# Performance work log

Measured on AMD Instinct MI355X. Metric: run time of the kernel, lower is better.

Reference implementation:

```python
import jax, jax.numpy as jnp
import numpy as np

B, K, N, D, H, NNEG, NTOP = 8, 8, 128, 256, 128, 64, 64
UNARY_SCALES = (1.0, 1.0, 1.0)  # one scale per tree level, tree_height = log2(K) = 3


def setup_inputs():
    key = jax.random.key(0)
    ks = jax.random.split(key, 8)
    s = 0.05
    return {
        'pos_fea': jax.random.normal(ks[0], (B, K, N, D), jnp.float32),
        'neg_fea': jax.random.normal(ks[1], (B * K, NNEG, D), jnp.float32),
        'pos_classes': jax.random.randint(ks[2], (B, K, N), 0, 20),
        'target_class': jax.random.randint(ks[3], (B,), 0, 20),
        'Wp1': jax.random.normal(ks[4], (2 * D, H), jnp.float32) * s,
        'bp1': jnp.zeros((H,), jnp.float32),
        'Wp2': jax.random.normal(ks[5], (H, 1), jnp.float32) * s,
        'bp2': jnp.zeros((1,), jnp.float32),
        'Wu1': jax.random.normal(ks[6], (2 * D, H), jnp.float32) * s,
        'bu1': jnp.zeros((H,), jnp.float32),
        'Wu2': jax.random.normal(ks[7], (H, 1), jnp.float32) * s,
        'bu2': jnp.zeros((1,), jnp.float32),
    }


def _relation(f0, f1, W1, b1, W2, b2):
    # RelationModule: Dense(H, relu) -> Dense(1) applied to concat([f0_m, f1_n])
    # for every cross pair; concat-Dense is split into two GEMMs. -> [Bn, M0, M1]
    d = f0.shape[-1]
    h0 = jnp.einsum('bmd,dh->bmh', f0, W1[:d])
    h1 = jnp.einsum('bnd,dh->bnh', f1, W1[d:])
    h = jax.nn.relu(h0[:, :, None, :] + h1[:, None, :, :] + b1)
    return jnp.einsum('bmnh,h->bmn', h, W2[:, 0]) + b2[0]


def _bg(t, idx):
    # batched_gather along axis 1: t [Bn, P, ...], idx [Bn, T]
    ie = idx.reshape(idx.shape + (1,) * (t.ndim - 2))
    ie = jnp.broadcast_to(ie, idx.shape + t.shape[2:])
    return jnp.take_along_axis(t, ie, axis=1)


def _rep(fea, sub):
    # subproblem representative feature: fea [Bn,S,N,D], sub [Bn,M,S] -> [Bn,M,D]
    idx = jnp.swapaxes(sub, 1, 2)[..., None]              # [Bn,S,M,1]
    idx = jnp.broadcast_to(idx, idx.shape[:-1] + (fea.shape[-1],))
    return jnp.take_along_axis(fea, idx, axis=2).mean(axis=1)


def _tree(pos_fea, neg_fea, Wp1, bp1, Wp2, bp2, Wu1, bu1, Wu2, bu2):
    pos_flat = pos_fea.reshape(B * K, N, D)
    # UnaryModule: mean relation score of each positive proposal vs the negative bag
    ue = _relation(pos_flat, neg_fea, Wu1, bu1, Wu2, bu2).mean(-1)   # [B*K, N]
    sub = jnp.broadcast_to(jnp.arange(N, dtype=jnp.int32)[None, :, None], (B * K, N, 1))
    pe = jnp.zeros_like(ue)
    tree_height = int(np.log2(K))
    best = None
    for i in range(tree_height):
        S = 2 ** i                      # subproblem size per branch at this level
        Bn = sub.shape[0] // 2
        M = sub.shape[1]
        sub2 = sub.reshape(Bn, 2, M, S)  # [::2] / [1::2] split of adjacent rows
        sub0, sub1 = sub2[:, 0], sub2[:, 1]
        pe2 = pe.reshape(Bn, 2, M)
        ue2 = ue.reshape(Bn, 2, M)
        fea = pos_flat.reshape(Bn, 2, S, N, D)
        rep0 = _rep(fea[:, 0], sub0)
        rep1 = _rep(fea[:, 1], sub1)
        # PairwiseCrossSimilarity: scores for all cross pairs of candidates
        scores = _relation(rep0, rep1, Wp1, bp1, Wp2, bp2).reshape(Bn, M * M)
        p0 = jnp.repeat(jnp.arange(M), M)
        p1 = jnp.tile(jnp.arange(M), M)
        pe = pe2[:, 0][:, p0] + pe2[:, 1][:, p1] - scores
        ue = ue2[:, 0][:, p0] + ue2[:, 1][:, p1]
        total = pe + UNARY_SCALES[i] * ue
        sub = jnp.concatenate([sub0[:, p0], sub1[:, p1]], axis=-1)  # [Bn, M*M, 2S]
        topk = 1 if i == tree_height - 1 else min(M * M, NTOP)
        _, inds = jax.lax.top_k(-total, topk)
        sub = _bg(sub, inds)
        ue = jnp.take_along_axis(ue, inds, axis=1)
        pe = jnp.take_along_axis(pe, inds, axis=1)
        best = jnp.take_along_axis(total, inds, axis=1)
    return sub, best


def reference(pos_fea, neg_fea, pos_classes, target_class,
              Wp1, bp1, Wp2, bp2, Wu1, bu1, Wu2, bu2):
    sub, _ = _tree(pos_fea, neg_fea, Wp1, bp1, Wp2, bp2, Wu1, bu1, Wu2, bu2)
    is_target = (pos_classes == target_class[:, None, None]).astype(jnp.float32)
    return sub[:, 0], is_target  # selected proposal per image [B,K], [B,K,N]
```

## Files before the change

kernel.cpp:

```cpp
#include <hip/hip_runtime.h>
#include <stdint.h>

#define B_ 8
#define K_ 8
#define N_ 128
#define D_ 256
#define H_ 128
#define NNEG_ 64

typedef unsigned long long u64;

__device__ __forceinline__ u64 shfl_xor_u64(u64 v, int m) {
    int lo = __shfl_xor((int)(unsigned)v, m, 64);
    int hi = __shfl_xor((int)(unsigned)(v >> 32), m, 64);
    return ((u64)(unsigned)hi << 32) | (unsigned)lo;
}
__device__ __forceinline__ u64 bitonic_merge64(u64 m, int lane) {
#pragma unroll
    for (int j = 32; j > 0; j >>= 1) {
        u64 o = shfl_xor_u64(m, j);
        bool keepMin = ((lane & j) == 0);
        bool lt = m < o;
        m = (keepMin == lt) ? m : o;
    }
    return m;
}
__device__ __forceinline__ u64 merge2(u64 a, u64 b, int lane) {
    u64 br = shfl_xor_u64(b, 63);
    u64 m = a < br ? a : br;
    return bitonic_merge64(m, lane);
}
__device__ __forceinline__ unsigned sortable(float f) {
    unsigned u = __float_as_uint(f);
    return (u & 0x80000000u) ? ~u : (u | 0x80000000u);
}
__device__ __forceinline__ float unsortable(unsigned u) {
    return __uint_as_float((u & 0x80000000u) ? (u & 0x7FFFFFFFu) : ~u);
}
__device__ __forceinline__ void sort128_reg(u64& v0, u64& v1, int lane) {
#pragma unroll
    for (int k = 2; k <= 64; k <<= 1) {
        bool d0 = ((lane & k) == 0);
        bool d1 = (k == 64) ? false : d0;
#pragma unroll
        for (int j = k >> 1; j > 0; j >>= 1) {
            u64 o0 = shfl_xor_u64(v0, j);
            bool km0 = (((lane & j) == 0) == d0);
            v0 = (km0 == (v0 < o0)) ? v0 : o0;
            u64 o1 = shfl_xor_u64(v1, j);
            bool km1 = (((lane & j) == 0) == d1);
            v1 = (km1 == (v1 < o1)) ? v1 : o1;
        }
    }
    if (v0 > v1) { u64 tmp = v0; v0 = v1; v1 = tmp; }
#pragma unroll
    for (int j = 32; j > 0; j >>= 1) {
        bool km = ((lane & j) == 0);
        u64 o0 = shfl_xor_u64(v0, j);
        v0 = (km == (v0 < o0)) ? v0 : o0;
        u64 o1 = shfl_xor_u64(v1, j);
        v1 = (km == (v1 < o1)) ? v1 : o1;
    }
}

__global__ __launch_bounds__(128) void g1_gemm(
    const float* __restrict__ pos, const float* __restrict__ neg,
    const float* __restrict__ Wu1, const float* __restrict__ Wp1,
    const int* __restrict__ pos_classes, const int* __restrict__ target_class,
    float* __restrict__ HU0, float* __restrict__ HU1n,
    float* __restrict__ HP0, float* __restrict__ HP1,
    float* __restrict__ outp) {
    int bid = blockIdx.x;
    int t = threadIdx.x;
    if (bid >= 896) {
        int base = (bid - 896) * 2048 + t * 16;
#pragma unroll
        for (int q = 0; q < 16; ++q) {
            int idx = base + q;
            outp[64 + idx] = (pos_classes[idx] == target_class[idx >> 10]) ? 1.0f : 0.0f;
        }
        return;
    }
    const float* A; const float* W; float* OUT; int bid2;
    if (bid < 256)      { A = pos; W = Wu1;           OUT = HU0;  bid2 = bid; }
    else if (bid < 384) { A = neg; W = Wu1 + D_ * H_; OUT = HU1n; bid2 = bid - 256; }
    else if (bid < 640) { A = pos; W = Wp1;           OUT = HP0;  bid2 = bid - 384; }
    else                { A = pos; W = Wp1 + D_ * H_; OUT = HP1;  bid2 = bid - 640; }
    int rb = (bid2 >> 1) * 64;
    int cb64 = (bid2 & 1) * 64;

    __shared__ float AsT[2][32][68];
    __shared__ float Bs[2][32][64];
    int tx = t & 7, ty = t >> 3;
    float acc[4][8];
#pragma unroll
    for (int i = 0; i < 4; ++i)
#pragma unroll
        for (int j = 0; j < 8; ++j) acc[i][j] = 0.f;

#pragma unroll
    for (int rep = 0; rep < 4; ++rep) {
        int flat = t + rep * 128;
        int row = flat >> 3, kq = flat & 7;
        const float4 av = *(const float4*)&A[(size_t)(rb + row) * D_ + kq * 4];
        AsT[0][kq * 4 + 0][row] = av.x;
        AsT[0][kq * 4 + 1][row] = av.y;
        AsT[0][kq * 4 + 2][row] = av.z;
        AsT[0][kq * 4 + 3][row] = av.w;
    }
#pragma unroll
    for (int rep = 0; rep < 4; ++rep) {
        int flat = t + rep * 128;
        int kr = flat >> 4, cq = flat & 15;
        *(float4*)&Bs[0][kr][cq * 4] =
            *(const float4*)&W[(size_t)kr * H_ + cb64 + cq * 4];
    }
    __syncthreads();

    for (int chunk = 0; chunk < 8; ++chunk) {
        int cur = chunk & 1, nxt = cur ^ 1;
        bool pre = (chunk < 7);
        int k0n = (chunk + 1) * 32;
        float4 pa[4], pb[4];
        if (pre) {
#pragma unroll
            for (int rep = 0; rep < 4; ++rep) {
                int flat = t + rep * 128;
                int row = flat >> 3, kq = flat & 7;
                pa[rep] = *(const float4*)&A[(size_t)(rb + row) * D_ + k0n + kq * 4];
            }
#pragma unroll
            for (int rep = 0; rep < 4; ++rep) {
                int flat = t + rep * 128;
                int kr = flat >> 4, cq = flat & 15;
                pb[rep] = *(const float4*)&W[(size_t)(k0n + kr) * H_ + cb64 + cq * 4];
            }
        }
#pragma unroll 8
        for (int kk = 0; kk < 32; ++kk) {
            const float4 av = *(const float4*)&AsT[cur][kk][ty * 4];
            float bv[8];
            *(float4*)&bv[0] = *(const float4*)&Bs[cur][kk][tx * 8];
            *(float4*)&bv[4] = *(const float4*)&Bs[cur][kk][tx * 8 + 4];
#pragma unroll
            for (int j = 0; j < 8; ++j) {
                acc[0][j] += av.x * bv[j];
                acc[1][j] += av.y * bv[j];
                acc[2][j] += av.z * bv[j];
                acc[3][j] += av.w * bv[j];
            }
        }
        if (pre) {
#pragma unroll
            for (int rep = 0; rep < 4; ++rep) {
                int flat = t + rep * 128;
                int row = flat >> 3, kq = flat & 7;
                AsT[nxt][kq * 4 + 0][row] = pa[rep].x;
                AsT[nxt][kq * 4 + 1][row] = pa[rep].y;
                AsT[nxt][kq * 4 + 2][row] = pa[rep].z;
                AsT[nxt][kq * 4 + 3][row] = pa[rep].w;
            }
#pragma unroll
            for (int rep = 0; rep < 4; ++rep) {
                int flat = t + rep * 128;
                int kr = flat >> 4, cq = flat & 15;
                *(float4*)&Bs[nxt][kr][cq * 4] = pb[rep];
            }
        }
        __syncthreads();
    }
#pragma unroll
    for (int i = 0; i < 4; ++i) {
        float4 o0 = {acc[i][0], acc[i][1], acc[i][2], acc[i][3]};
        float4 o1 = {acc[i][4], acc[i][5], acc[i][6], acc[i][7]};
        *(float4*)&OUT[(size_t)(rb + ty * 4 + i) * H_ + cb64 + tx * 8] = o0;
        *(float4*)&OUT[(size_t)(rb + ty * 4 + i) * H_ + cb64 + tx * 8 + 4] = o1;
    }
}

__global__ __launch_bounds__(256) void g2_ue_sc0(
    const float* __restrict__ HU0, const float* __restrict__ HU1n,
    const float* __restrict__ bu1, const float* __restrict__ Wu2,
    const float* __restrict__ bu2v,
    const float* __restrict__ HP0, const float* __restrict__ HP1,
    const float* __restrict__ bp1, const float* __restrict__ Wp2,
    const float* __restrict__ bp2,
    float* __restrict__ t0, float* __restrict__ sc0) {
    __shared__ float LsT[128][36];
    __shared__ float RsT[128][66];
    __shared__ float wsv[128];
    __shared__ float red[32][33];

    int bid = blockIdx.x;
    int t = threadIdx.x;
    bool is_ue = bid < 256;

    const float* Lsrc; const float* Rsrc; const float* b1v; const float* W2;
    if (is_ue) {
        int bk = bid >> 2, mt = bid & 3;
        Lsrc = HU0 + (size_t)(bk * N_ + mt * 32) * H_;
        Rsrc = HU1n + (size_t)bk * NNEG_ * H_;
        b1v = bu1; W2 = Wu2;
    } else {
        int bid2 = bid - 256;
        int b = bid2 >> 3, m0t = (bid2 >> 1) & 3, m1t = bid2 & 1;
        Lsrc = HP0 + (size_t)b * 2 * N_ * H_ + m0t * 32 * H_;
        Rsrc = HP1 + (size_t)b * 2 * N_ * H_ + N_ * H_ + m1t * 64 * H_;
        b1v = bp1; W2 = Wp2;
    }
    for (int i = t; i < 32 * 32; i += 256) {
        int m = i & 31, hq = i >> 5;
        const float4 a = *(const float4*)&Lsrc[(size_t)m * H_ + hq * 4];
        const float4 b = *(const float4*)&b1v[hq * 4];
        LsT[hq * 4 + 0][m] = a.x + b.x;
        LsT[hq * 4 + 1][m] = a.y + b.y;
        LsT[hq * 4 + 2][m] = a.z + b.z;
        LsT[hq * 4 + 3][m] = a.w + b.w;
    }
    for (int i = t; i < 64 * 32; i += 256) {
        int n = i & 63, hq = i >> 6;
        const float4 a = *(const float4*)&Rsrc[(size_t)n * H_ + hq * 4];
        RsT[hq * 4 + 0][n] = a.x;
        RsT[hq * 4 + 1][n] = a.y;
        RsT[hq * 4 + 2][n] = a.z;
        RsT[hq * 4 + 3][n] = a.w;
    }
    if (t < 128) wsv[t] = W2[t];
    __syncthreads();

    int tm = t & 7, tn = t >> 3;
    float a00 = 0.f, a01 = 0.f, a10 = 0.f, a11 = 0.f;
    float a20 = 0.f, a21 = 0.f, a30 = 0.f, a31 = 0.f;
#pragma unroll 4
    for (int h = 0; h < 128; ++h) {
        const float4 lv = *(const float4*)&LsT[h][tm * 4];
        const float2 rv = *(const float2*)&RsT[h][tn * 2];
        float w = wsv[h];
        float v;
        v = lv.x + rv.x; v = v > 0.f ? v : 0.f; a00 += v * w;
        v = lv.x + rv.y; v = v > 0.f ? v : 0.f; a01 += v * w;
        v = lv.y + rv.x; v = v > 0.f ? v : 0.f; a10 += v * w;
        v = lv.y + rv.y; v = v > 0.f ? v : 0.f; a11 += v * w;
        v = lv.z + rv.x; v = v > 0.f ? v : 0.f; a20 += v * w;
        v = lv.z + rv.y; v = v > 0.f ? v : 0.f; a21 += v * w;
        v = lv.w + rv.x; v = v > 0.f ? v : 0.f; a30 += v * w;
        v = lv.w + rv.y; v = v > 0.f ? v : 0.f; a31 += v * w;
    }

    if (is_ue) {
        int bk = bid >> 2, mt = bid & 3;
        red[tm * 4 + 0][tn] = a00 + a01;
        red[tm * 4 + 1][tn] = a10 + a11;
        red[tm * 4 + 2][tn] = a20 + a21;
        red[tm * 4 + 3][tn] = a30 + a31;
        __syncthreads();
        if (t < 32) {
            float s = 0.f;
            for (int q = 0; q < 32; ++q) s += red[t][q];
            t0[bk * N_ + mt * 32 + t] = s * (1.0f / NNEG_) + bu2v[0];
        }
    } else {
        int bid2 = bid - 256;
        int b = bid2 >> 3, m0t = (bid2 >> 1) & 3, m1t = bid2 & 1;
        float bp2v = bp2[0];
        float* orow = sc0 + (size_t)b * 16384;
        float accs[4][2] = {{a00, a01}, {a10, a11}, {a20, a21}, {a30, a31}};
#pragma unroll
        for (int i = 0; i < 4; ++i) {
            int m0 = m0t * 32 + tm * 4 + i;
#pragma unroll
            for (int j = 0; j < 2; ++j) {
                int m1 = m1t * 64 + tn * 2 + j;
                orow[m0 * 128 + m1] = accs[i][j] + bp2v;
            }
        }
    }
}

__global__ __launch_bounds__(256) void g3a_top0(const float* __restrict__ sc0,
                                                const float* __restrict__ t0,
                                                u64* __restrict__ g3c) {
    int bid = blockIdx.x;
    int r = bid >> 3, c = bid & 7;
    int t = threadIdx.x, lane = t & 63, w = t >> 6;
    __shared__ float tt[256];
    __shared__ u64 cand[4][128];
    if (t < 256) tt[t] = t0[r * 256 + t];
    __syncthreads();
    const float* row = sc0 + (size_t)r * 16384 + c * 2048 + w * 512;
    unsigned sv[8];
#pragma unroll
    for (int j = 0; j < 8; ++j) {
        int li = j * 64 + lane;
        int idx = c * 2048 + w * 512 + li;
        float v = (tt[idx >> 7] + tt[128 + (idx & 127)]) - row[li];
        sv[j] = sortable(v);
    }
    unsigned T = 0u;
#pragma unroll
    for (int it = 0; it < 16; ++it) {
        int p = 30 - 2 * it;
        unsigned C1 = T | (1u << p), C2 = T | (2u << p), C3 = T | (3u << p);
        unsigned c1 = 0u, c2 = 0u, c3 = 0u;
#pragma unroll
        for (int j = 0; j < 8; ++j) {
            c1 += (unsigned)__popcll(__ballot(sv[j] < C1));
            c2 += (unsigned)__popcll(__ballot(sv[j] < C2));
            c3 += (unsigned)__popcll(__ballot(sv[j] < C3));
        }
        unsigned k = (c3 < 64u) ? 3u : (c2 < 64u) ? 2u : (c1 < 64u) ? 1u : 0u;
        T |= (k << p);
    }
    u64* my = cand[w];
    int base = 0;
#pragma unroll
    for (int j = 0; j < 8; ++j) {
        u64 mask = __ballot(sv[j] <= T);
        if (sv[j] <= T) {
            int pos = base + (int)__popcll(mask & ((1ull << lane) - 1ull));
            if (pos < 128) {
                int idx = c * 2048 + w * 512 + j * 64 + lane;
                my[pos] = ((u64)sv[j] << 32) | (unsigned)idx;
            }
        }
        base += (int)__popcll(mask);
    }
    int cc = base < 128 ? base : 128;
    u64 v0 = (lane < cc) ? my[lane] : ~0ull;
    u64 v1 = (64 + lane < cc) ? my[64 + lane] : ~0ull;
    sort128_reg(v0, v1, lane);
    my[lane] = v0;
    __syncthreads();
    if (w == 0) {
        u64 x0 = cand[0][lane], x1 = cand[1][lane];
        u64 x2 = cand[2][lane], x3 = cand[3][lane];
        u64 y0 = merge2(x0, x1, lane), y1 = merge2(x2, x3, lane);
        g3c[(size_t)bid * 64 + lane] = merge2(y0, y1, lane);
    }
}

__global__ __launch_bounds__(256) void g4a_s1(
    const float* __restrict__ HP0, const float* __restrict__ HP1,
    const u64* __restrict__ g3c, int* __restrict__ pA,
    const float* __restrict__ bp1, const float* __restrict__ Wp2,
    const float* __restrict__ bp2, u64* __restrict__ g4top) {
    int bid = blockIdx.x;
    int u = bid >> 3, mq = (bid >> 1) & 3, nh = bid & 1;
    int t = threadIdx.x, lane = t & 63, w = t >> 6;
    __shared__ float LsT[128][17];
    __shared__ float RsT[128][34];
    __shared__ float taL[64], taR[64];
    __shared__ int paL[64], paR[64];
    __shared__ float wsv[128];
    __shared__ u64 cand[4][64];
    if (w < 2) {
        const u64* Lp = g3c + (size_t)(2 * u + w) * 512;
        u64 x0 = Lp[lane], x1 = Lp[64 + lane], x2 = Lp[128 + lane], x3 = Lp[192 + lane];
        u64 x4 = Lp[256 + lane], x5 = Lp[320 + lane], x6 = Lp[384 + lane], x7 = Lp[448 + lane];
        u64 y0 = merge2(x0, x1, lane), y1 = merge2(x2, x3, lane);
        u64 y2 = merge2(x4, x5, lane), y3 = merge2(x6, x7, lane);
        u64 z0 = merge2(y0, y1, lane), z1 = merge2(y2, y3, lane);
        u64 f = merge2(z0, z1, lane);
        int idx = (int)(f & 0xFFFFFFFFull);
        int pk = ((idx >> 7) << 8) | (idx & 127);
        float tv = unsortable((unsigned)(f >> 32));
        if (w == 0) { taL[lane] = tv; paL[lane] = pk; }
        else        { taR[lane] = tv; paR[lane] = pk; }
    }
    if (t >= 128) wsv[t - 128] = Wp2[t - 128];
    float bp2v = bp2[0];
    __syncthreads();
    if ((bid & 7) == 0) {
        if (t < 64) pA[(2 * u) * 64 + t] = paL[t];
        else if (t < 128) pA[(2 * u + 1) * 64 + (t - 64)] = paR[t - 64];
    }
    for (int i = t; i < 16 * 128; i += 256) {
        int m = i >> 7, h = i & 127;
        int pk = paL[mq * 16 + m]; int a0 = pk >> 8, a1 = pk & 255;
        float s = HP0[(size_t)(4 * u) * 16384 + a0 * 128 + h]
                + HP0[(size_t)(4 * u + 1) * 16384 + a1 * 128 + h];
        LsT[h][m] = s * 0.5f + bp1[h];
    }
    for (int i = t; i < 32 * 128; i += 256) {
        int n = i >> 7, h = i & 127;
        int pk = paR[nh * 32 + n]; int c0 = pk >> 8, c1 = pk & 255;
        float s = HP1[(size_t)(4 * u + 2) * 16384 + c0 * 128 + h]
                + HP1[(size_t)(4 * u + 3) * 16384 + c1 * 128 + h];
        RsT[h][n] = s * 0.5f;
    }
    __syncthreads();
    int lm = w * 4 + (lane >> 4);
    int ln = lane & 15;
    float a0 = 0.f, a1 = 0.f;
#pragma unroll 4
    for (int h = 0; h < 128; ++h) {
        float lv = LsT[h][lm];
        const float2 rv = *(const float2*)&RsT[h][ln * 2];
        float wv = wsv[h];
        float v;
        v = lv + rv.x; v = v > 0.f ? v : 0.f; a0 += v * wv;
        v = lv + rv.y; v = v > 0.f ? v : 0.f; a1 += v * wv;
    }
    int m_unit = mq * 16 + lm;
    int n0 = nh * 32 + ln * 2;
    float val0 = (taL[mq * 16 + lm] + taR[nh * 32 + ln * 2 + 0]) - (a0 + bp2v);
    float val1 = (taL[mq * 16 + lm] + taR[nh * 32 + ln * 2 + 1]) - (a1 + bp2v);
    u64 v0 = ((u64)sortable(val0) << 32) | (unsigned)(m_unit * 64 + n0);
    u64 v1 = ((u64)sortable(val1) << 32) | (unsigned)(m_unit * 64 + n0 + 1);
    sort128_reg(v0, v1, lane);
    cand[w][lane] = v0;
    __syncthreads();
    if (w == 0) {
        u64 x0 = cand[0][lane], x1 = cand[1][lane];
        u64 x2 = cand[2][lane], x3 = cand[3][lane];
        u64 y0 = merge2(x0, x1, lane), y1 = merge2(x2, x3, lane);
        g4top[(size_t)bid * 64 + lane] = merge2(y0, y1, lane);
    }
}

__global__ __launch_bounds__(256) void g4b_s2(
    const float* __restrict__ HP0, const float* __restrict__ HP1,
    const int* __restrict__ pA, const u64* __restrict__ g4top,
    const float* __restrict__ bp1, const float* __restrict__ Wp2,
    const float* __restrict__ bp2, float* __restrict__ outp) {
    int b = blockIdx.x;
    int t = threadIdx.x, lane = t & 63, w = t >> 6;
    __shared__ float LsT[128][68];
    __shared__ float RsT[128][36];
    __shared__ float tL[64], tR[64];
    __shared__ unsigned subL[64], subR[64];
    __shared__ float wsv[128];
    __shared__ u64 sred[4];
    if (t < 128) wsv[t] = Wp2[t];
    float bp2v = bp2[0];
    if (w < 2) {
        const u64* Lp = g4top + (size_t)(2 * b + w) * 512;
        u64 x0 = Lp[lane], x1 = Lp[64 + lane], x2 = Lp[128 + lane], x3 = Lp[192 + lane];
        u64 x4 = Lp[256 + lane], x5 = Lp[320 + lane], x6 = Lp[384 + lane], x7 = Lp[448 + lane];
        u64 y0 = merge2(x0, x1, lane), y1 = merge2(x2, x3, lane);
        u64 y2 = merge2(x4, x5, lane), y3 = merge2(x6, x7, lane);
        u64 z0 = merge2(y0, y1, lane), z1 = merge2(y2, y3, lane);
        u64 m = merge2(z0, z1, lane);
        int idx = (int)(m & 0xFFFFFFFFull);
        int p0 = idx >> 6, p1 = idx & 63;
        float val = unsortable((unsigned)(m >> 32));
        int rowL = 4 * b + 2 * w;
        int pkL = pA[rowL * 64 + p0];
        int pkR = pA[(rowL + 1) * 64 + p1];
        unsigned leaves = ((unsigned)pkL << 16) | (unsigned)pkR;
        if (w == 0) { tL[lane] = val; subL[lane] = leaves; }
        else        { tR[lane] = val; subR[lane] = leaves; }
    }
    __syncthreads();
    for (int i = t; i < 64 * 128; i += 256) {
        int m = i >> 7, h = i & 127;
        unsigned s4 = subL[m];
        float s = HP0[(size_t)(8 * b + 0) * 16384 + ((s4 >> 24) & 255u) * 128 + h]
                + HP0[(size_t)(8 * b + 1) * 16384 + ((s4 >> 16) & 255u) * 128 + h]
                + HP0[(size_t)(8 * b + 2) * 16384 + ((s4 >> 8) & 255u) * 128 + h]
                + HP0[(size_t)(8 * b + 3) * 16384 + (s4 & 255u) * 128 + h];
        LsT[h][m] = s * 0.25f + bp1[h];
    }
    u64 best = ~0ull;
    int qm = w * 4 + (lane >> 4);
    int qn = lane & 15;
    for (int half = 0; half < 2; ++half) {
        __syncthreads();
        for (int i = t; i < 32 * 128; i += 256) {
            int n = i >> 7, h = i & 127;
            int ng = half * 32 + n;
            unsigned s4 = subR[ng];
            float s = HP1[(size_t)(8 * b + 4) * 16384 + ((s4 >> 24) & 255u) * 128 + h]
                    + HP1[(size_t)(8 * b + 5) * 16384 + ((s4 >> 16) & 255u) * 128 + h]
                    + HP1[(size_t)(8 * b + 6) * 16384 + ((s4 >> 8) & 255u) * 128 + h]
                    + HP1[(size_t)(8 * b + 7) * 16384 + (s4 & 255u) * 128 + h];
            RsT[h][n] = s * 0.25f;
        }
        __syncthreads();
        float acc[4][2];
#pragma unroll
        for (int i = 0; i < 4; ++i) { acc[i][0] = 0.f; acc[i][1] = 0.f; }
#pragma unroll 2
        for (int h = 0; h < 128; ++h) {
            const float4 lv = *(const float4*)&LsT[h][qm * 4];
            const float2 rv = *(const float2*)&RsT[h][qn * 2];
            float wv = wsv[h];
            float v;
            v = lv.x + rv.x; v = v > 0.f ? v : 0.f; acc[0][0] += v * wv;
            v = lv.x + rv.y; v = v > 0.f ? v : 0.f; acc[0][1] += v * wv;
            v = lv.y + rv.x; v = v > 0.f ? v : 0.f; acc[1][0] += v * wv;
            v = lv.y + rv.y; v = v > 0.f ? v : 0.f; acc[1][1] += v * wv;
            v = lv.z + rv.x; v = v > 0.f ? v : 0.f; acc[2][0] += v * wv;
            v = lv.z + rv.y; v = v > 0.f ? v : 0.f; acc[2][1] += v * wv;
            v = lv.w + rv.x; v = v > 0.f ? v : 0.f; acc[3][0] += v * wv;
            v = lv.w + rv.y; v = v > 0.f ? v : 0.f; acc[3][1] += v * wv;
        }
#pragma unroll
        for (int mi = 0; mi < 4; ++mi) {
#pragma unroll
            for (int nj = 0; nj < 2; ++nj) {
                int m = qm * 4 + mi;
                int ng = half * 32 + qn * 2 + nj;
                float val = (tL[m] + tR[ng]) - (acc[mi][nj] + bp2v);
                u64 kk = ((u64)sortable(val) << 32) | (unsigned)(m * 64 + ng);
                best = kk < best ? kk : best;
            }
        }
    }
#pragma unroll
    for (int off = 32; off > 0; off >>= 1) {
        u64 o = shfl_xor_u64(best, off);
        best = o < best ? o : best;
    }
    if (lane == 0) sred[w] = best;
    __syncthreads();
    if (t == 0) {
        u64 bb = sred[0];
        for (int p = 1; p < 4; ++p) { u64 o = sred[p]; bb = o < bb ? o : bb; }
        int idx = (int)(bb & 0xFFFFFFFFull);
        unsigned sl = subL[idx >> 6], sr = subR[idx & 63];
        outp[b * 8 + 0] = (float)((sl >> 24) & 255u);
        outp[b * 8 + 1] = (float)((sl >> 16) & 255u);
        outp[b * 8 + 2] = (float)((sl >> 8) & 255u);
        outp[b * 8 + 3] = (float)(sl & 255u);
        outp[b * 8 + 4] = (float)((sr >> 24) & 255u);
        outp[b * 8 + 5] = (float)((sr >> 16) & 255u);
        outp[b * 8 + 6] = (float)((sr >> 8) & 255u);
        outp[b * 8 + 7] = (float)(sr & 255u);
    }
}

extern "C" void kernel_launch(void* const* d_in, const int* in_sizes, int n_in,
                              void* d_out, int out_size, void* d_ws, size_t ws_size,
                              hipStream_t stream) {
    const float* pos = (const float*)d_in[0];
    const float* neg = (const float*)d_in[1];
    const int* pos_classes = (const int*)d_in[2];
    const int* target_class = (const int*)d_in[3];
    const float* Wp1 = (const float*)d_in[4];
    const float* bp1 = (const float*)d_in[5];
    const float* Wp2 = (const float*)d_in[6];
    const float* bp2 = (const float*)d_in[7];
    const float* Wu1 = (const float*)d_in[8];
    const float* bu1 = (const float*)d_in[9];
    const float* Wu2 = (const float*)d_in[10];
    const float* bu2 = (const float*)d_in[11];

    float* wsf = (float*)d_ws;
    float* HU0 = wsf;
    float* HP0 = HU0 + 1048576;
    float* HP1 = HP0 + 1048576;
    float* HU1n = HP1 + 1048576;
    float* t0 = HU1n + 524288;
    float* sc0 = t0 + 8192;
    int* pA = (int*)(sc0 + 524288);
    u64* g3c = (u64*)wsf;
    u64* g4top = (u64*)wsf + 16384;
    float* outp = (float*)d_out;

    g1_gemm<<<900, 128, 0, stream>>>(pos, neg, Wu1, Wp1, pos_classes,
                                     target_class, HU0, HU1n, HP0, HP1, outp);
    g2_ue_sc0<<<512, 256, 0, stream>>>(HU0, HU1n, bu1, Wu2, bu2,
                                       HP0, HP1, bp1, Wp2, bp2, t0, sc0);
    g3a_top0<<<256, 256, 0, stream>>>(sc0, t0, g3c);
    g4a_s1<<<128, 256, 0, stream>>>(HP0, HP1, g3c, pA, bp1, Wp2, bp2, g4top);
    g4b_s2<<<8, 256, 0, stream>>>(HP0, HP1, pA, g4top, bp1, Wp2, bp2, outp);
}
```

Baseline: 173.1 us.

## Stream GEMM weights through registers and enlarge per-thread tiles in relation kernel

In the projection GEMM, the weight matrix is no longer staged in shared memory. Each thread loads its 8 weight columns straight from global memory into registers with a one-step prefetch, and the A tile is now kept row-major and read as float4 vectors. In the pairwise relu-score kernel the block shrinks to 128 threads, each computing a 4x4 output tile with vectorized LDS reads and vectorized stores. The aim is less LDS traffic and fewer barriers per FMA, at the cost of more global load instructions and register pressure.

```diff
diff --git a/kernel.cpp b/kernel.cpp
--- a/kernel.cpp
+++ b/kernel.cpp
@@ -9,6 +9,7 @@
 #define NNEG_ 64
 
 typedef unsigned long long u64;
+typedef float f4 __attribute__((ext_vector_type(4)));
 
 __device__ __forceinline__ u64 shfl_xor_u64(u64 v, int m) {
     int lo = __shfl_xor((int)(unsigned)v, m, 64);
@@ -89,96 +90,89 @@
     int rb = (bid2 >> 1) * 64;
     int cb64 = (bid2 & 1) * 64;
 
-    __shared__ float AsT[2][32][68];
-    __shared__ float Bs[2][32][64];
+    __shared__ float As[2][64][36];
     int tx = t & 7, ty = t >> 3;
-    float acc[4][8];
-#pragma unroll
-    for (int i = 0; i < 4; ++i)
-#pragma unroll
-        for (int j = 0; j < 8; ++j) acc[i][j] = 0.f;
+    f4 acc[4][2];
+#pragma unroll
+    for (int i = 0; i < 4; ++i) { acc[i][0] = (f4)0.f; acc[i][1] = (f4)0.f; }
+
+    const float* Wb = W + cb64 + tx * 8;
 
 #pragma unroll
     for (int rep = 0; rep < 4; ++rep) {
         int flat = t + rep * 128;
         int row = flat >> 3, kq = flat & 7;
-        const float4 av = *(const float4*)&A[(size_t)(rb + row) * D_ + kq * 4];
-        AsT[0][kq * 4 + 0][row] = av.x;
-        AsT[0][kq * 4 + 1][row] = av.y;
-        AsT[0][kq * 4 + 2][row] = av.z;
-        AsT[0][kq * 4 + 3][row] = av.w;
-    }
-#pragma unroll
-    for (int rep = 0; rep < 4; ++rep) {
-        int flat = t + rep * 128;
-        int kr = flat >> 4, cq = flat & 15;
-        *(float4*)&Bs[0][kr][cq * 4] =
-            *(const float4*)&W[(size_t)kr * H_ + cb64 + cq * 4];
+        *(f4*)&As[0][row][kq * 4] = *(const f4*)&A[(size_t)(rb + row) * D_ + kq * 4];
+    }
+    f4 bcur[4][2], bnxt[4][2];
+#pragma unroll
+    for (int q = 0; q < 4; ++q) {
+        bcur[q][0] = *(const f4*)&Wb[(size_t)q * H_];
+        bcur[q][1] = *(const f4*)&Wb[(size_t)q * H_ + 4];
     }
     __syncthreads();
 
     for (int chunk = 0; chunk < 8; ++chunk) {
         int cur = chunk & 1, nxt = cur ^ 1;
         bool pre = (chunk < 7);
-        int k0n = (chunk + 1) * 32;
-        float4 pa[4], pb[4];
+        f4 pa[4];
         if (pre) {
+            int k0n = (chunk + 1) * 32;
 #pragma unroll
             for (int rep = 0; rep < 4; ++rep) {
                 int flat = t + rep * 128;
                 int row = flat >> 3, kq = flat & 7;
-                pa[rep] = *(const float4*)&A[(size_t)(rb + row) * D_ + k0n + kq * 4];
-            }
-#pragma unroll
-            for (int rep = 0; rep < 4; ++rep) {
-                int flat = t + rep * 128;
-                int kr = flat >> 4, cq = flat & 15;
-                pb[rep] = *(const float4*)&W[(size_t)(k0n + kr) * H_ + cb64 + cq * 4];
-            }
-        }
-#pragma unroll 8
-        for (int kk = 0; kk < 32; ++kk) {
-            const float4 av = *(const float4*)&AsT[cur][kk][ty * 4];
-            float bv[8];
-            *(float4*)&bv[0] = *(const float4*)&Bs[cur][kk][tx * 8];
-            *(float4*)&bv[4] = *(const float4*)&Bs[cur][kk][tx * 8 + 4];
-#pragma unroll
-            for (int j = 0; j < 8; ++j) {
-                acc[0][j] += av.x * bv[j];
-                acc[1][j] += av.y * bv[j];
-                acc[2][j] += av.z * bv[j];
-                acc[3][j] += av.w * bv[j];
-            }
+                pa[rep] = *(const f4*)&A[(size_t)(rb + row) * D_ + k0n + kq * 4];
+            }
+        }
+#pragma unroll
+        for (int g = 0; g < 8; ++g) {
+            int kg = chunk * 8 + g;
+            if (kg + 1 < 64) {
+                int kb = (kg + 1) * 4;
+#pragma unroll
+                for (int q = 0; q < 4; ++q) {
+                    bnxt[q][0] = *(const f4*)&Wb[(size_t)(kb + q) * H_];
+                    bnxt[q][1] = *(const f4*)&Wb[(size_t)(kb + q) * H_ + 4];
+                }
+            }
+            f4 av[4];
+#pragma unroll
+            for (int i = 0; i < 4; ++i)
+                av[i] = *(const f4*)&As[cur][ty * 4 + i][g * 4];
+#pragma unroll
+            for (int q = 0; q < 4; ++q) {
+                f4 b0 = bcur[q][0], b1 = bcur[q][1];
+#pragma unroll
+                for (int i = 0; i < 4; ++i) {
+                    float a = av[i][q];
+                    acc[i][0][0] += a * b0[0]; acc[i][0][1] += a * b0[1];
+                    acc[i][0][2] += a * b0[2]; acc[i][0][3] += a * b0[3];
+                    acc[i][1][0] += a * b1[0]; acc[i][1][1] += a * b1[1];
+                    acc[i][1][2] += a * b1[2]; acc[i][1][3] += a * b1[3];
+                }
+            }
+#pragma unroll
+            for (int q = 0; q < 4; ++q) { bcur[q][0] = bnxt[q][0]; bcur[q][1] = bnxt[q][1]; }
         }
         if (pre) {
 #pragma unroll
             for (int rep = 0; rep < 4; ++rep) {
                 int flat = t + rep * 128;
                 int row = flat >> 3, kq = flat & 7;
-                AsT[nxt][kq * 4 + 0][row] = pa[rep].x;
-                AsT[nxt][kq * 4 + 1][row] = pa[rep].y;
-                AsT[nxt][kq * 4 + 2][row] = pa[rep].z;
-                AsT[nxt][kq * 4 + 3][row] = pa[rep].w;
-            }
-#pragma unroll
-            for (int rep = 0; rep < 4; ++rep) {
-                int flat = t + rep * 128;
-                int kr = flat >> 4, cq = flat & 15;
-                *(float4*)&Bs[nxt][kr][cq * 4] = pb[rep];
+                *(f4*)&As[nxt][row][kq * 4] = pa[rep];
             }
         }
         __syncthreads();
     }
 #pragma unroll
     for (int i = 0; i < 4; ++i) {
-        float4 o0 = {acc[i][0], acc[i][1], acc[i][2], acc[i][3]};
-        float4 o1 = {acc[i][4], acc[i][5], acc[i][6], acc[i][7]};
-        *(float4*)&OUT[(size_t)(rb + ty * 4 + i) * H_ + cb64 + tx * 8] = o0;
-        *(float4*)&OUT[(size_t)(rb + ty * 4 + i) * H_ + cb64 + tx * 8 + 4] = o1;
-    }
-}
-
-__global__ __launch_bounds__(256) void g2_ue_sc0(
+        *(f4*)&OUT[(size_t)(rb + ty * 4 + i) * H_ + cb64 + tx * 8] = acc[i][0];
+        *(f4*)&OUT[(size_t)(rb + ty * 4 + i) * H_ + cb64 + tx * 8 + 4] = acc[i][1];
+    }
+}
+
+__global__ __launch_bounds__(128) void g2_ue_sc0(
     const float* __restrict__ HU0, const float* __restrict__ HU1n,
     const float* __restrict__ bu1, const float* __restrict__ Wu2,
     const float* __restrict__ bu2v,
@@ -187,7 +181,7 @@
     const float* __restrict__ bp2,
     float* __restrict__ t0, float* __restrict__ sc0) {
     __shared__ float LsT[128][36];
-    __shared__ float RsT[128][66];
+    __shared__ float RsT[128][68];
     __shared__ float wsv[128];
     __shared__ float red[32][33];
 
@@ -208,51 +202,61 @@
         Rsrc = HP1 + (size_t)b * 2 * N_ * H_ + N_ * H_ + m1t * 64 * H_;
         b1v = bp1; W2 = Wp2;
     }
-    for (int i = t; i < 32 * 32; i += 256) {
+    for (int i = t; i < 32 * 32; i += 128) {
         int m = i & 31, hq = i >> 5;
-        const float4 a = *(const float4*)&Lsrc[(size_t)m * H_ + hq * 4];
-        const float4 b = *(const float4*)&b1v[hq * 4];
-        LsT[hq * 4 + 0][m] = a.x + b.x;
-        LsT[hq * 4 + 1][m] = a.y + b.y;
-        LsT[hq * 4 + 2][m] = a.z + b.z;
-        LsT[hq * 4 + 3][m] = a.w + b.w;
-    }
-    for (int i = t; i < 64 * 32; i += 256) {
+        const f4 a = *(const f4*)&Lsrc[(size_t)m * H_ + hq * 4];
+        const f4 b = *(const f4*)&b1v[hq * 4];
+        LsT[hq * 4 + 0][m] = a[0] + b[0];
+        LsT[hq * 4 + 1][m] = a[1] + b[1];
+        LsT[hq * 4 + 2][m] = a[2] + b[2];
+        LsT[hq * 4 + 3][m] = a[3] + b[3];
+    }
+    for (int i = t; i < 64 * 32; i += 128) {
         int n = i & 63, hq = i >> 6;
-        const float4 a = *(const float4*)&Rsrc[(size_t)n * H_ + hq * 4];
-        RsT[hq * 4 + 0][n] = a.x;
-        RsT[hq * 4 + 1][n] = a.y;
-        RsT[hq * 4 + 2][n] = a.z;
-        RsT[hq * 4 + 3][n] = a.w;
-    }
-    if (t < 128) wsv[t] = W2[t];
+        const f4 a = *(const f4*)&Rsrc[(size_t)n * H_ + hq * 4];
+        RsT[hq * 4 + 0][n] = a[0];
+        RsT[hq * 4 + 1][n] = a[1];
+        RsT[hq * 4 + 2][n] = a[2];
+        RsT[hq * 4 + 3][n] = a[3];
+    }
+    wsv[t] = W2[t];
     __syncthreads();
 
     int tm = t & 7, tn = t >> 3;
-    float a00 = 0.f, a01 = 0.f, a10 = 0.f, a11 = 0.f;
-    float a20 = 0.f, a21 = 0.f, a30 = 0.f, a31 = 0.f;
-#pragma unroll 4
-    for (int h = 0; h < 128; ++h) {
-        const float4 lv = *(const float4*)&LsT[h][tm * 4];
-        const float2 rv = *(const float2*)&RsT[h][tn * 2];
-        float w = wsv[h];
-        float v;
-        v = lv.x + rv.x; v = v > 0.f ? v : 0.f; a00 += v * w;
-        v = lv.x + rv.y; v = v > 0.f ? v : 0.f; a01 += v * w;
-        v = lv.y + rv.x; v = v > 0.f ? v : 0.f; a10 += v * w;
-        v = lv.y + rv.y; v = v > 0.f ? v : 0.f; a11 += v * w;
-        v = lv.z + rv.x; v = v > 0.f ? v : 0.f; a20 += v * w;
-        v = lv.z + rv.y; v = v > 0.f ? v : 0.f; a21 += v * w;
-        v = lv.w + rv.x; v = v > 0.f ? v : 0.f; a30 += v * w;
-        v = lv.w + rv.y; v = v > 0.f ? v : 0.f; a31 += v * w;
+    f4 acc[4];
+#pragma unroll
+    for (int i = 0; i < 4; ++i) acc[i] = (f4)0.f;
+#pragma unroll 2
+    for (int hg = 0; hg < 32; ++hg) {
+        f4 wv = *(const f4*)&wsv[hg * 4];
+        f4 lv[4], rv[4];
+#pragma unroll
+        for (int s = 0; s < 4; ++s) {
+            lv[s] = *(const f4*)&LsT[hg * 4 + s][tm * 4];
+            rv[s] = *(const f4*)&RsT[hg * 4 + s][tn * 4];
+        }
+#pragma unroll
+        for (int s = 0; s < 4; ++s) {
+            float w = wv[s];
+#pragma unroll
+            for (int i = 0; i < 4; ++i) {
+                float l = lv[s][i];
+                float v;
+                v = l + rv[s][0]; v = v > 0.f ? v : 0.f; acc[i][0] += v * w;
+                v = l + rv[s][1]; v = v > 0.f ? v : 0.f; acc[i][1] += v * w;
+                v = l + rv[s][2]; v = v > 0.f ? v : 0.f; acc[i][2] += v * w;
+                v = l + rv[s][3]; v = v > 0.f ? v : 0.f; acc[i][3] += v * w;
+            }
+        }
     }
 
     if (is_ue) {
         int bk = bid >> 2, mt = bid & 3;
-        red[tm * 4 + 0][tn] = a00 + a01;
-        red[tm * 4 + 1][tn] = a10 + a11;
-        red[tm * 4 + 2][tn] = a20 + a21;
-        red[tm * 4 + 3][tn] = a30 + a31;
+#pragma unroll
+        for (int i = 0; i < 4; ++i) {
+            red[tm * 4 + i][tn * 2 + 0] = acc[i][0] + acc[i][1];
+            red[tm * 4 + i][tn * 2 + 1] = acc[i][2] + acc[i][3];
+        }
         __syncthreads();
         if (t < 32) {
             float s = 0.f;
@@ -264,15 +268,13 @@
         int b = bid2 >> 3, m0t = (bid2 >> 1) & 3, m1t = bid2 & 1;
         float bp2v = bp2[0];
         float* orow = sc0 + (size_t)b * 16384;
-        float accs[4][2] = {{a00, a01}, {a10, a11}, {a20, a21}, {a30, a31}};
 #pragma unroll
         for (int i = 0; i < 4; ++i) {
             int m0 = m0t * 32 + tm * 4 + i;
-#pragma unroll
-            for (int j = 0; j < 2; ++j) {
-                int m1 = m1t * 64 + tn * 2 + j;
-                orow[m0 * 128 + m1] = accs[i][j] + bp2v;
-            }
+            int m1 = m1t * 64 + tn * 4;
+            f4 o = {acc[i][0] + bp2v, acc[i][1] + bp2v,
+                    acc[i][2] + bp2v, acc[i][3] + bp2v};
+            *(f4*)&orow[m0 * 128 + m1] = o;
         }
     }
 }
@@ -560,7 +562,7 @@
 
     g1_gemm<<<900, 128, 0, stream>>>(pos, neg, Wu1, Wp1, pos_classes,
                                      target_class, HU0, HU1n, HP0, HP1, outp);
-    g2_ue_sc0<<<512, 256, 0, stream>>>(HU0, HU1n, bu1, Wu2, bu2,
+    g2_ue_sc0<<<512, 128, 0, stream>>>(HU0, HU1n, bu1, Wu2, bu2,
                                        HP0, HP1, bp1, Wp2, bp2, t0, sc0);
     g3a_top0<<<256, 256, 0, stream>>>(sc0, t0, g3c);
     g4a_s1<<<128, 256, 0, stream>>>(HP0, HP1, g3c, pA, bp1, Wp2, bp2, g4top);
```

After: 194.3 us. 12.2% more time.
